# Kernel optimization log

Measured on AMD Instinct MI355X. Metric: run time of the kernel, lower is better.

Reference implementation:

```python
import jax, jax.numpy as jnp
import numpy as np

N, E, F, H = 20000, 320000, 128, 256   # nodes, edges, in-features, hidden
M, NQ = 4096, 2048                      # lsq rows, QP variables
LAMB_MAX = 2.0


def setup_inputs() -> dict:
    key = jax.random.key(0)
    ks = jax.random.split(key, 12)
    x = jax.random.normal(ks[0], (N, F), jnp.float32)
    edge_index = jax.random.randint(ks[1], (2, E), 0, N)
    A = jax.random.normal(ks[2], (M, NQ), jnp.float32) * 0.05
    b = jax.random.normal(ks[3], (M, 1), jnp.float32)
    feat_ids = jax.random.randint(ks[4], (NQ,), 0, N)
    x_prior = jax.random.uniform(ks[5], (NQ, 1), jnp.float32)
    lamb = jnp.ones((1,), jnp.float32)
    # ChebConv K=2 weights: one linear per Chebyshev order, plus bias
    W10 = jax.random.normal(ks[6], (F, H), jnp.float32) / np.sqrt(F)
    W11 = jax.random.normal(ks[7], (F, H), jnp.float32) / np.sqrt(F)
    b1 = jnp.zeros((H,), jnp.float32)
    W20 = jax.random.normal(ks[8], (H, 1), jnp.float32) / np.sqrt(H)
    W21 = jax.random.normal(ks[9], (H, 1), jnp.float32) / np.sqrt(H)
    b2 = jnp.zeros((1,), jnp.float32)
    return {"x": x, "edge_index": edge_index, "A": A, "b": b,
            "feat_ids": feat_ids, "x_prior": x_prior, "lamb": lamb,
            "W10": W10, "W11": W11, "b1": b1,
            "W20": W20, "W21": W21, "b2": b2}


def _cheb_conv(x, edge_index, W0, W1, bias, lam_max):
    """PyG ChebConv with K=2: out = x @ W0 + (2L/lam_max - I) x @ W1 + bias,
    L = I - D^{-1/2} A D^{-1/2}, via edge gather/scatter (no dense NxN)."""
    row, col = edge_index[0], edge_index[1]
    n = x.shape[0]
    deg = jax.ops.segment_sum(jnp.ones_like(row, dtype=x.dtype), row, num_segments=n)
    dinv = jnp.where(deg > 0, deg ** -0.5, 0.0)
    # normalized edge weight scaled by 2/lam_max, negated (off-diag of L_hat)
    w = -(2.0 / lam_max) * dinv[row] * dinv[col]              # [E]
    msg = jax.ops.segment_sum(w[:, None] * x[col], row, num_segments=n)
    Tx1 = msg + (2.0 / lam_max - 1.0) * x                      # diagonal of L_hat
    return x @ W0 + Tx1 @ W1 + bias


def reference(x, edge_index, A, b, feat_ids, x_prior, lamb,
              W10, W11, b1, W20, W21, b2):
    h = jax.nn.relu(_cheb_conv(x, edge_index, W10, W11, b1, LAMB_MAX))
    h = lamb[0] * jax.nn.relu(_cheb_conv(h, edge_index, W20, W21, b2, LAMB_MAX))
    hfold = h[feat_ids] + 1e-5                                 # [NQ, 1]
    q = hfold[:, 0]
    # QP: min 1/2 z^T Q z + p^T z with vacuous inequality (0*z <= 0.1) and no
    # equality constraints -> interior-point converges to unconstrained min.
    Q = A.T @ A + jnp.diag(q)                                  # [NQ, NQ]
    p = -(x_prior * hfold)[:, 0] - (b.T @ A)[0]                # [NQ]
    z = jnp.linalg.solve(Q, -p)                                # [NQ]
    return z[:, None]                                          # f.T -> [NQ, 1]
```

## Files before the change

### kernel.cpp

```cpp
#include <hip/hip_runtime.h>

#define N_NODES 20000
#define N_EDGES 320000
#define F_DIM   128
#define H_DIM   256
#define M_ROWS  4096
#define NQ      2048
#define NIT     18
#define MM_ROWS 20032

typedef __attribute__((ext_vector_type(8))) short short8;
typedef __attribute__((ext_vector_type(4))) float f32x4;


__device__ __forceinline__ float wred(float v) {
#pragma unroll
  for (int m = 32; m > 0; m >>= 1) v += __shfl_xor(v, m, 64);
  return v;
}

__device__ __forceinline__ float bred256(float v, float* lds) {
  v = wred(v);
  int w = threadIdx.x >> 6;
  if ((threadIdx.x & 63) == 0) lds[w] = v;
  __syncthreads();
  float tot = lds[0] + lds[1] + lds[2] + lds[3];
  __syncthreads();
  return tot;
}

__device__ __forceinline__ unsigned f2bf(float f) {
  unsigned u = __float_as_uint(f);
  unsigned r = u + 0x7fffu + ((u >> 16) & 1u);
  return r >> 16;
}
__device__ __forceinline__ float bflo(unsigned u) { return __uint_as_float(u << 16); }
__device__ __forceinline__ float bfhi(unsigned u) { return __uint_as_float(u & 0xffff0000u); }


__global__ __launch_bounds__(256) void k_deg(const int* __restrict__ ei, int* __restrict__ deg) {
  int e = blockIdx.x * 256 + threadIdx.x;
  if (e < N_EDGES) atomicAdd(&deg[ei[e]], 1);
}

__global__ __launch_bounds__(1024) void k_scan(const int* __restrict__ deg,
    int* __restrict__ rowstart, float* __restrict__ dinv) {
  __shared__ int part[1024];
  int t = threadIdx.x;
  const int chunk = (N_NODES + 1023) / 1024;
  int lo = t * chunk;
  int hi = lo + chunk; if (hi > N_NODES) hi = N_NODES;
  int s = 0;
  for (int i = lo; i < hi; ++i) {
    int d = deg[i];
    dinv[i] = d > 0 ? rsqrtf((float)d) : 0.f;
    s += d;
  }
  part[t] = s;
  __syncthreads();
  for (int off = 1; off < 1024; off <<= 1) {
    int v = part[t];
    int add = (t >= off) ? part[t - off] : 0;
    __syncthreads();
    part[t] = v + add;
    __syncthreads();
  }
  int base = (t > 0) ? part[t - 1] : 0;
  for (int i = lo; i < hi; ++i) { rowstart[i] = base; base += deg[i]; }
  if (t == 0) rowstart[N_NODES] = part[1023];
}

__global__ __launch_bounds__(256) void k_scatter(const int* __restrict__ ei,
    const int* __restrict__ rowstart, int* __restrict__ cursor,
    const float* __restrict__ dinv, int* __restrict__ cols, float* __restrict__ wvals) {
  int e = blockIdx.x * 256 + threadIdx.x;
  if (e >= N_EDGES) return;
  int r = ei[e];
  int c = ei[N_EDGES + e];
  int pos = rowstart[r] + atomicAdd(&cursor[r], 1);
  cols[pos] = c;
  wvals[pos] = -dinv[r] * dinv[c];
}

#define CONVX_BLKS (MM_ROWS * 16 / 256)

__global__ __launch_bounds__(256) void k_pack(const float* __restrict__ x,
    const float* __restrict__ W10, const float* __restrict__ W11,
    unsigned* __restrict__ xu, unsigned* __restrict__ Wtb) {
  int bx = blockIdx.x;
  if (bx < CONVX_BLKS) {
    int gid = bx * 256 + threadIdx.x;
    int row = gid >> 4;
    int q8 = gid & 15;
    uint4* xu4 = (uint4*)xu;
    if (row < N_NODES) {
      const float4* x4 = (const float4*)x;
      float4 a = x4[(size_t)row * 32 + q8 * 2];
      float4 b = x4[(size_t)row * 32 + q8 * 2 + 1];
      uint4 u;
      u.x = f2bf(a.x) | (f2bf(a.y) << 16);
      u.y = f2bf(a.z) | (f2bf(a.w) << 16);
      u.z = f2bf(b.x) | (f2bf(b.y) << 16);
      u.w = f2bf(b.z) | (f2bf(b.w) << 16);
      xu4[(size_t)row * 32 + q8] = u;
    } else {
      uint4 z = make_uint4(0, 0, 0, 0);
      xu4[(size_t)row * 32 + q8] = z;
      xu4[(size_t)row * 32 + 16 + q8] = z;
    }
  } else {
    int gid = (bx - CONVX_BLKS) * 256 + threadIdx.x;
    int n = gid >> 7;
    int u = gid & 127;
    int k0 = u * 2;
    float v0 = (k0 < 128) ? W10[(size_t)k0 * H_DIM + n]
                          : W11[(size_t)(k0 - 128) * H_DIM + n];
    float v1 = (k0 + 1 < 128) ? W10[(size_t)(k0 + 1) * H_DIM + n]
                              : W11[(size_t)(k0 - 127) * H_DIM + n];
    Wtb[(size_t)n * 128 + u] = f2bf(v0) | (f2bf(v1) << 16);
  }
}

__global__ __launch_bounds__(256) void k_msg1(const int* __restrict__ rowstart,
    const int* __restrict__ cols, const float* __restrict__ wvals,
    unsigned* __restrict__ xu) {
  int wid = (blockIdx.x * 256 + threadIdx.x) >> 6;
  int lane = threadIdx.x & 63;
  if (wid >= N_NODES) return;
  int s0 = rowstart[wid], s1 = rowstart[wid + 1];
  float2 acc = make_float2(0.f, 0.f);
  for (int e = s0; e < s1; ++e) {
    int c = cols[e];
    float w = wvals[e];
    unsigned u = xu[(size_t)c * 128 + lane];
    acc.x += w * bflo(u);
    acc.y += w * bfhi(u);
  }
  xu[(size_t)wid * 128 + 64 + lane] = f2bf(acc.x) | (f2bf(acc.y) << 16);
}


__device__ __forceinline__ void mm_ldfrag(short8* Af, short8* Bf,
    const unsigned* __restrict__ xurow, const unsigned* __restrict__ wrow, int kc) {
#pragma unroll
  for (int a = 0; a < 4; ++a)
    Af[a] = *(const short8*)(xurow + (size_t)a * 16 * 128 + kc * 16);
#pragma unroll
  for (int n = 0; n < 4; ++n)
    Bf[n] = *(const short8*)(wrow + (size_t)n * 16 * 128 + kc * 16);
}

__global__ __launch_bounds__(256) void k_mm(const unsigned* __restrict__ xu,
    const unsigned* __restrict__ Wtb, const float* __restrict__ b1,
    const float* __restrict__ W20, const float* __restrict__ W21,
    float* __restrict__ t, float* __restrict__ s) {
  const int row0 = blockIdx.x * 64;
  const int tid = threadIdx.x;
  const int w = tid >> 6, lane = tid & 63;
  const int colb = w * 64;
  const int frow = lane & 15, fqo = (lane >> 4) * 4;
  const int c16 = lane & 15, q4 = lane >> 4;

  f32x4 acc[4][4];
#pragma unroll
  for (int a = 0; a < 4; ++a)
#pragma unroll
    for (int b = 0; b < 4; ++b) {
      acc[a][b][0] = 0.f; acc[a][b][1] = 0.f;
      acc[a][b][2] = 0.f; acc[a][b][3] = 0.f;
    }

  const unsigned* xurow = xu + (size_t)(row0 + frow) * 128 + fqo;
  const unsigned* wrow  = Wtb + (size_t)(colb + frow) * 128 + fqo;

  short8 A0[4], B0[4], A1[4], B1[4];
  mm_ldfrag(A0, B0, xurow, wrow, 0);
#pragma unroll
  for (int kp = 0; kp < 4; ++kp) {
    const int kc = kp * 2;
    mm_ldfrag(A1, B1, xurow, wrow, kc + 1);
#pragma unroll
    for (int a = 0; a < 4; ++a)
#pragma unroll
      for (int n = 0; n < 4; ++n)
        acc[a][n] = __builtin_amdgcn_mfma_f32_16x16x32_bf16(A0[a], B0[n], acc[a][n], 0, 0, 0);
    if (kc + 2 < 8) mm_ldfrag(A0, B0, xurow, wrow, kc + 2);
#pragma unroll
    for (int a = 0; a < 4; ++a)
#pragma unroll
      for (int n = 0; n < 4; ++n)
        acc[a][n] = __builtin_amdgcn_mfma_f32_16x16x32_bf16(A1[a], B1[n], acc[a][n], 0, 0, 0);
  }

  float tp[4][4] = {}, sp[4][4] = {};
#pragma unroll
  for (int b2 = 0; b2 < 4; ++b2) {
    int gc = colb + b2 * 16 + c16;
    float w20 = W20[gc], w21 = W21[gc], bb = b1[gc];
#pragma unroll
    for (int a = 0; a < 4; ++a)
#pragma unroll
      for (int r = 0; r < 4; ++r) {
        float val = acc[a][b2][r] + bb;
        val = val > 0.f ? val : 0.f;
        tp[a][r] += val * w20;
        sp[a][r] += val * w21;
      }
  }
#pragma unroll
  for (int a = 0; a < 4; ++a)
#pragma unroll
    for (int r = 0; r < 4; ++r) {
#pragma unroll
      for (int m = 1; m < 16; m <<= 1) {
        tp[a][r] += __shfl_xor(tp[a][r], m, 64);
        sp[a][r] += __shfl_xor(sp[a][r], m, 64);
      }
    }
  if (c16 == 0) {
#pragma unroll
    for (int a = 0; a < 4; ++a)
#pragma unroll
      for (int r = 0; r < 4; ++r) {
        int gr = row0 + a * 16 + q4 * 4 + r;
        if (gr < N_NODES) {
          atomicAdd(&t[gr], tp[a][r]);
          atomicAdd(&s[gr], sp[a][r]);
        }
      }
  }
}


__global__ __launch_bounds__(256) void k_h2(const float* __restrict__ t,
    const float* __restrict__ s, const int* __restrict__ rowstart,
    const int* __restrict__ cols, const float* __restrict__ wvals,
    const float* __restrict__ lamb, const float* __restrict__ b2, float* __restrict__ h2) {
  int i = blockIdx.x * 256 + threadIdx.x;
  if (i >= N_NODES) return;
  float m = 0.f;
  int s0 = rowstart[i], s1 = rowstart[i + 1];
  for (int e = s0; e < s1; ++e) m += wvals[e] * s[cols[e]];
  float val = t[i] + m + b2[0];
  val = val > 0.f ? val : 0.f;
  h2[i] = lamb[0] * val;
}

__global__ __launch_bounds__(256) void k_prep(const float* __restrict__ A,
    const float* __restrict__ b, unsigned* __restrict__ Atu, float* __restrict__ btA_parts) {
  int jp = blockIdx.x * 256 + threadIdx.x;
  int k0 = blockIdx.y * 128;
  const float2* A2 = (const float2*)A;
  float acc0 = 0.f, acc1 = 0.f;
  for (int kk = 0; kk < 128; kk += 8) {
    float ax[8], ay[8];
#pragma unroll
    for (int i = 0; i < 8; ++i) {
      int k = k0 + kk + i;
      float2 a = A2[(size_t)k * 1024 + jp];
      float bk = b[k];
      acc0 += a.x * bk;
      acc1 += a.y * bk;
      ax[i] = a.x; ay[i] = a.y;
    }
    uint4 t0, t1;
    t0.x = f2bf(ax[0]) | (f2bf(ax[1]) << 16);
    t0.y = f2bf(ax[2]) | (f2bf(ax[3]) << 16);
    t0.z = f2bf(ax[4]) | (f2bf(ax[5]) << 16);
    t0.w = f2bf(ax[6]) | (f2bf(ax[7]) << 16);
    t1.x = f2bf(ay[0]) | (f2bf(ay[1]) << 16);
    t1.y = f2bf(ay[2]) | (f2bf(ay[3]) << 16);
    t1.z = f2bf(ay[4]) | (f2bf(ay[5]) << 16);
    t1.w = f2bf(ay[6]) | (f2bf(ay[7]) << 16);
    int uoff = (k0 + kk) >> 1;
    *(uint4*)(Atu + (size_t)(2 * jp) * 2048 + uoff) = t0;
    *(uint4*)(Atu + (size_t)(2 * jp + 1) * 2048 + uoff) = t1;
  }
  ((float2*)(btA_parts + (size_t)blockIdx.y * NQ))[jp] = make_float2(acc0, acc1);
}

__global__ __launch_bounds__(256) void k_qrhs(const float* __restrict__ h2,
    const int* __restrict__ feat_ids, const float* __restrict__ x_prior,
    const float* __restrict__ btA_parts, float* __restrict__ q, float* __restrict__ r) {
  int j = blockIdx.x * 256 + threadIdx.x;
  int f = feat_ids[j];
  float hf = h2[f] + 1e-5f;
  q[j] = hf;
  float bta = 0.f;
#pragma unroll
  for (int c = 0; c < 32; ++c) bta += btA_parts[(size_t)c * NQ + j];
  r[j] = x_prior[j] * hf + bta;
}

#define GR_ST 20
#define NTILE 136

__global__ __launch_bounds__(512) void k_gram(const unsigned* __restrict__ Atu,
                                              float* __restrict__ Gp) {
  __shared__ unsigned shA[128 * GR_ST];
  __shared__ unsigned shB[128 * GR_ST];
  const int bid = blockIdx.x;
  const int wid = (bid & 7) * 68 + (bid >> 3);
  const int tile = wid >> 2;
  const int kq = wid & 3;
  int uu = tile, bi = 0;
  while (uu >= 16 - bi) { uu -= 16 - bi; ++bi; }
  const int bj = bi + uu;
  const int i0 = bi * 128, j0 = bj * 128;
  const int tid = threadIdx.x;
  const int w = tid >> 6, lane = tid & 63;
  const int wr = (w >> 2) * 64, wc = (w & 3) * 32;
  const int srow = tid >> 2, suo = (tid & 3) * 4;
  const int frow = lane & 15, fqo = (lane >> 4) * 4;

  f32x4 acc[4][2];
#pragma unroll
  for (int a = 0; a < 4; ++a)
#pragma unroll
    for (int b = 0; b < 2; ++b) {
      acc[a][b][0] = 0.f; acc[a][b][1] = 0.f;
      acc[a][b][2] = 0.f; acc[a][b][3] = 0.f;
    }

  const unsigned* pa = Atu + (size_t)(i0 + srow) * 2048 + kq * 512 + suo;
  const unsigned* pb = Atu + (size_t)(j0 + srow) * 2048 + kq * 512 + suo;

  uint4 ra0 = *(const uint4*)(pa);
  uint4 rb0 = *(const uint4*)(pb);
  uint4 ra1 = *(const uint4*)(pa + 16);
  uint4 rb1 = *(const uint4*)(pb + 16);

  unsigned* as = shA + srow * GR_ST + suo;
  unsigned* bs = shB + srow * GR_ST + suo;

  for (int sp = 0; sp < 16; ++sp) {
    *(uint4*)as = ra0;
    *(uint4*)bs = rb0;
    if (sp < 15) {
      const int ku = (2 * sp + 2) * 16;
      ra0 = *(const uint4*)(pa + ku);
      rb0 = *(const uint4*)(pb + ku);
    }
    __syncthreads();
    {
      short8 af[4], bf[2];
#pragma unroll
      for (int a = 0; a < 4; ++a)
        af[a] = *(const short8*)(shA + (wr + a * 16 + frow) * GR_ST + fqo);
#pragma unroll
      for (int b2 = 0; b2 < 2; ++b2)
        bf[b2] = *(const short8*)(shB + (wc + b2 * 16 + frow) * GR_ST + fqo);
#pragma unroll
      for (int a = 0; a < 4; ++a)
#pragma unroll
        for (int b2 = 0; b2 < 2; ++b2)
          acc[a][b2] = __builtin_amdgcn_mfma_f32_16x16x32_bf16(af[a], bf[b2], acc[a][b2], 0, 0, 0);
    }
    __syncthreads();
    *(uint4*)as = ra1;
    *(uint4*)bs = rb1;
    if (sp < 15) {
      const int ku = (2 * sp + 3) * 16;
      ra1 = *(const uint4*)(pa + ku);
      rb1 = *(const uint4*)(pb + ku);
    }
    __syncthreads();
    {
      short8 af[4], bf[2];
#pragma unroll
      for (int a = 0; a < 4; ++a)
        af[a] = *(const short8*)(shA + (wr + a * 16 + frow) * GR_ST + fqo);
#pragma unroll
      for (int b2 = 0; b2 < 2; ++b2)
        bf[b2] = *(const short8*)(shB + (wc + b2 * 16 + frow) * GR_ST + fqo);
#pragma unroll
      for (int a = 0; a < 4; ++a)
#pragma unroll
        for (int b2 = 0; b2 < 2; ++b2)
          acc[a][b2] = __builtin_amdgcn_mfma_f32_16x16x32_bf16(af[a], bf[b2], acc[a][b2], 0, 0, 0);
    }
    __syncthreads();
  }

  const int q4 = lane >> 4, c16 = lane & 15;
  float* Gz = Gp + ((size_t)kq * NTILE + tile) * 16384;
#pragma unroll
  for (int a = 0; a < 4; ++a)
#pragma unroll
    for (int b2 = 0; b2 < 2; ++b2)
#pragma unroll
      for (int r = 0; r < 4; ++r) {
        int lr = wr + a * 16 + q4 * 4 + r;
        int lc = wc + b2 * 16 + c16;
        Gz[lr * 128 + lc] = acc[a][b2][r];
      }
}

#define GT_ST 131

__global__ __launch_bounds__(256) void k_gconv(const float* __restrict__ Gp,
    const float* __restrict__ q, unsigned* __restrict__ Gb, float* __restrict__ qcorr) {
  __shared__ unsigned short T[128 * GT_ST];
  int uu = blockIdx.x, bi = 0;
  while (uu >= 16 - bi) { uu -= 16 - bi; ++bi; }
  const int bj = bi + uu;
  const int tid = threadIdx.x;
  const int r = tid >> 1, ch = (tid & 1) * 64;
  const size_t tile = (size_t)blockIdx.x * 16384;
  const float4* P0 = (const float4*)(Gp + tile + r * 128 + ch);
  const float4* P1 = (const float4*)(Gp + (size_t)1 * NTILE * 16384 + tile + r * 128 + ch);
  const float4* P2 = (const float4*)(Gp + (size_t)2 * NTILE * 16384 + tile + r * 128 + ch);
  const float4* P3 = (const float4*)(Gp + (size_t)3 * NTILE * 16384 + tile + r * 128 + ch);
  const int gr = bi * 128 + r;
  const bool hasdiag = (bi == bj) && (r >= ch) && (r < ch + 64);
  unsigned uo[32];
#pragma unroll
  for (int j = 0; j < 16; ++j) {
    float4 a = P0[j], b = P1[j], c = P2[j], d = P3[j];
    float v0 = a.x + b.x + c.x + d.x;
    float v1 = a.y + b.y + c.y + d.y;
    float v2 = a.z + b.z + c.z + d.z;
    float v3 = a.w + b.w + c.w + d.w;
    const int c0 = ch + j * 4;
    if (hasdiag && (r - c0 >= 0) && (r - c0 < 4)) {
      float qv = q[gr];
      int dsel = r - c0;
      if (dsel == 0) v0 += qv;
      else if (dsel == 1) v1 += qv;
      else if (dsel == 2) v2 += qv;
      else v3 += qv;
      float vd = (dsel == 0) ? v0 : (dsel == 1) ? v1 : (dsel == 2) ? v2 : v3;
      qcorr[gr] = vd - bflo(f2bf(vd));
    }
    unsigned u0 = f2bf(v0) | (f2bf(v1) << 16);
    unsigned u1 = f2bf(v2) | (f2bf(v3) << 16);
    uo[2 * j] = u0;
    uo[2 * j + 1] = u1;
    T[r * GT_ST + c0]     = (unsigned short)(u0 & 0xffffu);
    T[r * GT_ST + c0 + 1] = (unsigned short)(u0 >> 16);
    T[r * GT_ST + c0 + 2] = (unsigned short)(u1 & 0xffffu);
    T[r * GT_ST + c0 + 3] = (unsigned short)(u1 >> 16);
  }
  uint4* dst = (uint4*)(Gb + (size_t)gr * 1024 + bj * 64 + (ch >> 1));
#pragma unroll
  for (int j = 0; j < 8; ++j) dst[j] = ((const uint4*)uo)[j];
  __syncthreads();
  if (bi != bj) {
    const int wv = tid >> 6, lane = tid & 63;
    for (int kk = 0; kk < 32; ++kk) {
      int rr = kk * 4 + wv;
      unsigned lo = T[(2 * lane) * GT_ST + rr];
      unsigned hi = T[(2 * lane + 1) * GT_ST + rr];
      Gb[(size_t)(bj * 128 + rr) * 1024 + bi * 64 + lane] = lo | (hi << 16);
    }
  }
}

__global__ __launch_bounds__(256) void k_cgG(int k, const unsigned* __restrict__ Gb,
    const float* __restrict__ qcorr,
    const float* __restrict__ r_old, float* __restrict__ r_new,
    const float* __restrict__ p_old, float* __restrict__ p_new,
    const float* __restrict__ Qp_in, float* __restrict__ Qp_out,
    float* __restrict__ xcg) {
  __shared__ float pshare[NQ];
  __shared__ float lds[4];
  const int tid = threadIdx.x, bid = blockIdx.x;
  const float4* r4 = (const float4*)r_old;
  float4 ra = r4[tid * 2], rb2 = r4[tid * 2 + 1];
  float pv[8];
  if (k == 0) {
    pv[0] = ra.x; pv[1] = ra.y; pv[2] = ra.z; pv[3] = ra.w;
    pv[4] = rb2.x; pv[5] = rb2.y; pv[6] = rb2.z; pv[7] = rb2.w;
    if (bid == 0) {
      ((float4*)p_new)[tid * 2] = ra;
      ((float4*)p_new)[tid * 2 + 1] = rb2;
    }
  } else {
    const float4* p4 = (const float4*)p_old;
    const float4* qp4 = (const float4*)Qp_in;
    float4 pa = p4[tid * 2], pb = p4[tid * 2 + 1];
    float4 qa = qp4[tid * 2], qb = qp4[tid * 2 + 1];
    float rr = ra.x * ra.x + ra.y * ra.y + ra.z * ra.z + ra.w * ra.w +
               rb2.x * rb2.x + rb2.y * rb2.y + rb2.z * rb2.z + rb2.w * rb2.w;
    float pap = pa.x * qa.x + pa.y * qa.y + pa.z * qa.z + pa.w * qa.w +
                pb.x * qb.x + pb.y * qb.y + pb.z * qb.z + pb.w * qb.w;
    rr = bred256(rr, lds);
    pap = bred256(pap, lds);
    float alpha = rr / pap;
    if (bid == 0) {
      float4* x4 = (float4*)xcg;
      float4 xa = x4[tid * 2], xb = x4[tid * 2 + 1];
      xa.x += alpha * pa.x; xa.y += alpha * pa.y;
      xa.z += alpha * pa.z; xa.w += alpha * pa.w;
      xb.x += alpha * pb.x; xb.y += alpha * pb.y;
      xb.z += alpha * pb.z; xb.w += alpha * pb.w;
      x4[tid * 2] = xa; x4[tid * 2 + 1] = xb;
    }
    ra.x -= alpha * qa.x; ra.y -= alpha * qa.y;
    ra.z -= alpha * qa.z; ra.w -= alpha * qa.w;
    rb2.x -= alpha * qb.x; rb2.y -= alpha * qb.y;
    rb2.z -= alpha * qb.z; rb2.w -= alpha * qb.w;
    float rrn = ra.x * ra.x + ra.y * ra.y + ra.z * ra.z + ra.w * ra.w +
                rb2.x * rb2.x + rb2.y * rb2.y + rb2.z * rb2.z + rb2.w * rb2.w;
    rrn = bred256(rrn, lds);
    float beta = rrn / rr;
    pv[0] = ra.x + beta * pa.x; pv[1] = ra.y + beta * pa.y;
    pv[2] = ra.z + beta * pa.z; pv[3] = ra.w + beta * pa.w;
    pv[4] = rb2.x + beta * pb.x; pv[5] = rb2.y + beta * pb.y;
    pv[6] = rb2.z + beta * pb.z; pv[7] = rb2.w + beta * pb.w;
    if (bid == 0) {
      ((float4*)r_new)[tid * 2] = ra;
      ((float4*)r_new)[tid * 2 + 1] = rb2;
      ((float4*)p_new)[tid * 2] = make_float4(pv[0], pv[1], pv[2], pv[3]);
      ((float4*)p_new)[tid * 2 + 1] = make_float4(pv[4], pv[5], pv[6], pv[7]);
    }
  }
  ((float4*)pshare)[tid * 2] = make_float4(pv[0], pv[1], pv[2], pv[3]);
  ((float4*)pshare)[tid * 2 + 1] = make_float4(pv[4], pv[5], pv[6], pv[7]);
  __syncthreads();
  const int w = tid >> 6, lane = tid & 63;
  const int row0 = bid * 8 + w * 2;
  const uint4* Gr0 = (const uint4*)(Gb + (size_t)row0 * 1024);
  const uint4* Gr1 = (const uint4*)(Gb + (size_t)(row0 + 1) * 1024);
  const float4* ps4 = (const float4*)pshare;
  float acc0 = 0.f, acc1 = 0.f;
#pragma unroll
  for (int c = 0; c < 4; ++c) {
    uint4 g0 = Gr0[c * 64 + lane];
    uint4 g1 = Gr1[c * 64 + lane];
    float4 pa = ps4[c * 128 + lane * 2];
    float4 pb = ps4[c * 128 + lane * 2 + 1];
    acc0 += bflo(g0.x) * pa.x + bfhi(g0.x) * pa.y;
    acc0 += bflo(g0.y) * pa.z + bfhi(g0.y) * pa.w;
    acc0 += bflo(g0.z) * pb.x + bfhi(g0.z) * pb.y;
    acc0 += bflo(g0.w) * pb.z + bfhi(g0.w) * pb.w;
    acc1 += bflo(g1.x) * pa.x + bfhi(g1.x) * pa.y;
    acc1 += bflo(g1.y) * pa.z + bfhi(g1.y) * pa.w;
    acc1 += bflo(g1.z) * pb.x + bfhi(g1.z) * pb.y;
    acc1 += bflo(g1.w) * pb.z + bfhi(g1.w) * pb.w;
  }
  acc0 = wred(acc0);
  acc1 = wred(acc1);
  if (lane == 0) {
    Qp_out[row0] = acc0 + qcorr[row0] * pshare[row0];
    Qp_out[row0 + 1] = acc1 + qcorr[row0 + 1] * pshare[row0 + 1];
  }
}

__global__ __launch_bounds__(256) void k_cgfin(const float* __restrict__ r_last,
    const float* __restrict__ p_last, const float* __restrict__ Qp,
    const float* __restrict__ xcg, float* __restrict__ out) {
  const int tid = threadIdx.x;
  const int lane = tid & 63;
  const float4* r4 = (const float4*)r_last;
  const float4* p4 = (const float4*)p_last;
  const float4* q4 = (const float4*)Qp;
  float rr = 0.f, pap = 0.f;
#pragma unroll
  for (int c = 0; c < 4; ++c) {
#pragma unroll
    for (int hh = 0; hh < 2; ++hh) {
      float4 rv = r4[c * 128 + lane * 2 + hh];
      float4 pv = p4[c * 128 + lane * 2 + hh];
      float4 qv = q4[c * 128 + lane * 2 + hh];
      rr += rv.x * rv.x + rv.y * rv.y + rv.z * rv.z + rv.w * rv.w;
      pap += pv.x * qv.x + pv.y * qv.y + pv.z * qv.z + pv.w * qv.w;
    }
  }
  rr = wred(rr);
  pap = wred(pap);
  float alpha = rr / pap;
  const float4* x4 = (const float4*)xcg;
  float4* o4 = (float4*)out;
#pragma unroll
  for (int hh = 0; hh < 2; ++hh) {
    int i4 = tid * 2 + hh;
    float4 xv = x4[i4];
    float4 pv = p4[i4];
    xv.x += alpha * pv.x; xv.y += alpha * pv.y;
    xv.z += alpha * pv.z; xv.w += alpha * pv.w;
    o4[i4] = xv;
  }
}


extern "C" void kernel_launch(void* const* d_in, const int* in_sizes, int n_in,
                              void* d_out, int out_size, void* d_ws, size_t ws_size,
                              hipStream_t stream) {
  const float* x      = (const float*)d_in[0];
  const int*   ei     = (const int*)d_in[1];
  const float* A      = (const float*)d_in[2];
  const float* b      = (const float*)d_in[3];
  const int*   fids   = (const int*)d_in[4];
  const float* xprior = (const float*)d_in[5];
  const float* lamb   = (const float*)d_in[6];
  const float* W10    = (const float*)d_in[7];
  const float* W11    = (const float*)d_in[8];
  const float* b1     = (const float*)d_in[9];
  const float* W20    = (const float*)d_in[10];
  const float* W21    = (const float*)d_in[11];
  const float* b2     = (const float*)d_in[12];
  float* out = (float*)d_out;

  char* base = (char*)d_ws;
  size_t o = 0;
  auto alloc = [&](size_t bytes) { size_t r = o; o = (o + bytes + 255) & ~size_t(255); return r; };

  size_t off_deg    = alloc(N_NODES * 4);
  size_t off_cursor = alloc(N_NODES * 4);
  size_t off_xcg    = alloc(NQ * 4);
  size_t off_t      = alloc(N_NODES * 4);
  size_t off_s      = alloc(N_NODES * 4);
  size_t zero_end   = o;
  size_t off_rowst  = alloc((N_NODES + 1) * 4);
  size_t off_dinv   = alloc(N_NODES * 4);
  size_t off_h2     = alloc(N_NODES * 4);
  size_t off_q      = alloc(NQ * 4);
  size_t off_r0     = alloc(NQ * 4);
  size_t off_r1     = alloc(NQ * 4);
  size_t off_p0     = alloc(NQ * 4);
  size_t off_p1     = alloc(NQ * 4);
  size_t off_Qp0    = alloc(NQ * 4);
  size_t off_Qp1    = alloc(NQ * 4);
  size_t off_qcorr  = alloc(NQ * 4);
  size_t off_btAp   = alloc(32 * NQ * 4);
  size_t off_Wtb    = alloc(256 * 128 * 4);
  size_t sz_cols  = (size_t)N_EDGES * 4 + 256;
  size_t sz_wvals = (size_t)N_EDGES * 4 + 256;
  size_t sz_xmsg  = (size_t)MM_ROWS * 256 * 2;
  size_t union_gnn = sz_cols + sz_wvals + sz_xmsg;
  size_t union_at  = (size_t)M_ROWS * NQ * 2;
  size_t off_union = alloc(union_gnn > union_at ? union_gnn : union_at);
  size_t off_Gp    = alloc((size_t)4 * NTILE * 16384 * 4);
  if (o > ws_size) return;

  int*   deg      = (int*)(base + off_deg);
  int*   cursor   = (int*)(base + off_cursor);
  float* xcg      = (float*)(base + off_xcg);
  float* t        = (float*)(base + off_t);
  float* s        = (float*)(base + off_s);
  int*   rowstart = (int*)(base + off_rowst);
  float* dinv     = (float*)(base + off_dinv);
  float* h2       = (float*)(base + off_h2);
  float* q        = (float*)(base + off_q);
  float* rb[2]    = {(float*)(base + off_r0), (float*)(base + off_r1)};
  float* pg[2]    = {(float*)(base + off_p0), (float*)(base + off_p1)};
  float* Qpb[2]   = {(float*)(base + off_Qp0), (float*)(base + off_Qp1)};
  float* qcorr    = (float*)(base + off_qcorr);
  float* btA_parts = (float*)(base + off_btAp);
  unsigned* Wtb   = (unsigned*)(base + off_Wtb);
  int*   cols     = (int*)(base + off_union);
  float* wvals    = (float*)(base + off_union + sz_cols);
  unsigned* xmsgb = (unsigned*)(base + off_union + sz_cols + sz_wvals);
  unsigned* Atu   = (unsigned*)(base + off_union);
  unsigned* Gb    = (unsigned*)(base + off_union);
  float* Gp       = (float*)(base + off_Gp);

  hipMemsetAsync(d_ws, 0, zero_end, stream);

  k_deg<<<(N_EDGES + 255) / 256, 256, 0, stream>>>(ei, deg);
  k_scan<<<1, 1024, 0, stream>>>(deg, rowstart, dinv);
  k_scatter<<<(N_EDGES + 255) / 256, 256, 0, stream>>>(ei, rowstart, cursor, dinv, cols, wvals);

  k_pack<<<CONVX_BLKS + 128, 256, 0, stream>>>(x, W10, W11, xmsgb, Wtb);
  k_msg1<<<N_NODES / 4, 256, 0, stream>>>(rowstart, cols, wvals, xmsgb);
  k_mm<<<MM_ROWS / 64, 256, 0, stream>>>(xmsgb, Wtb, b1, W20, W21, t, s);
  k_h2<<<(N_NODES + 255) / 256, 256, 0, stream>>>(t, s, rowstart, cols, wvals, lamb, b2, h2);

  k_prep<<<dim3(4, 32), 256, 0, stream>>>(A, b, Atu, btA_parts);
  k_qrhs<<<NQ / 256, 256, 0, stream>>>(h2, fids, xprior, btA_parts, q, rb[0]);
  k_gram<<<544, 512, 0, stream>>>(Atu, Gp);
  k_gconv<<<NTILE, 256, 0, stream>>>(Gp, q, Gb, qcorr);

  k_cgG<<<256, 256, 0, stream>>>(0, Gb, qcorr, rb[0], rb[0], pg[0], pg[0],
                                 Qpb[1], Qpb[0], xcg);
  for (int k = 1; k < NIT; ++k) {
    k_cgG<<<256, 256, 0, stream>>>(k, Gb, qcorr, rb[(k - 1) & 1], rb[k & 1],
                                   pg[(k - 1) & 1], pg[k & 1],
                                   Qpb[(k - 1) & 1], Qpb[k & 1], xcg);
  }
  k_cgfin<<<1, 256, 0, stream>>>(rb[(NIT - 1) & 1], pg[(NIT - 1) & 1],
                                 Qpb[(NIT - 1) & 1], xcg, out);
}
```

Measured before the change: 406.2 us.

## Fuse CG iteration kernels into one cooperative persistent kernel with grid sync

Replaces the 18 per-iteration CG kernel launches and the final update launch with a single cooperative kernel. It loops over the iterations internally and uses grid-wide synchronization between them. The goal is to remove per-launch overhead and the gaps between dependent small kernels. In exchange, each iteration pays for a grid barrier plus a thread fence, which on AMD GPUs can cost about as much as a launch boundary.

```diff
diff --git a/kernel.cpp b/kernel.cpp
--- a/kernel.cpp
+++ b/kernel.cpp
@@ -1,4 +1,7 @@
 #include <hip/hip_runtime.h>
+#include <hip/hip_cooperative_groups.h>
+
+namespace cg = cooperative_groups;
 
 #define N_NODES 20000
 #define N_EDGES 320000
@@ -456,130 +459,144 @@
   }
 }
 
-__global__ __launch_bounds__(256) void k_cgG(int k, const unsigned* __restrict__ Gb,
+__global__ __launch_bounds__(256) void k_cg_all(const unsigned* __restrict__ Gb,
     const float* __restrict__ qcorr,
-    const float* __restrict__ r_old, float* __restrict__ r_new,
-    const float* __restrict__ p_old, float* __restrict__ p_new,
-    const float* __restrict__ Qp_in, float* __restrict__ Qp_out,
-    float* __restrict__ xcg) {
+    float* __restrict__ r0b, float* __restrict__ r1b,
+    float* __restrict__ p0b, float* __restrict__ p1b,
+    float* __restrict__ q0b, float* __restrict__ q1b,
+    float* __restrict__ xcg, float* __restrict__ out) {
+  cg::grid_group grid = cg::this_grid();
   __shared__ float pshare[NQ];
   __shared__ float lds[4];
   const int tid = threadIdx.x, bid = blockIdx.x;
-  const float4* r4 = (const float4*)r_old;
-  float4 ra = r4[tid * 2], rb2 = r4[tid * 2 + 1];
-  float pv[8];
-  if (k == 0) {
-    pv[0] = ra.x; pv[1] = ra.y; pv[2] = ra.z; pv[3] = ra.w;
-    pv[4] = rb2.x; pv[5] = rb2.y; pv[6] = rb2.z; pv[7] = rb2.w;
-    if (bid == 0) {
-      ((float4*)p_new)[tid * 2] = ra;
-      ((float4*)p_new)[tid * 2 + 1] = rb2;
-    }
-  } else {
-    const float4* p4 = (const float4*)p_old;
-    const float4* qp4 = (const float4*)Qp_in;
-    float4 pa = p4[tid * 2], pb = p4[tid * 2 + 1];
-    float4 qa = qp4[tid * 2], qb = qp4[tid * 2 + 1];
-    float rr = ra.x * ra.x + ra.y * ra.y + ra.z * ra.z + ra.w * ra.w +
-               rb2.x * rb2.x + rb2.y * rb2.y + rb2.z * rb2.z + rb2.w * rb2.w;
-    float pap = pa.x * qa.x + pa.y * qa.y + pa.z * qa.z + pa.w * qa.w +
-                pb.x * qb.x + pb.y * qb.y + pb.z * qb.z + pb.w * qb.w;
-    rr = bred256(rr, lds);
-    pap = bred256(pap, lds);
-    float alpha = rr / pap;
-    if (bid == 0) {
-      float4* x4 = (float4*)xcg;
-      float4 xa = x4[tid * 2], xb = x4[tid * 2 + 1];
-      xa.x += alpha * pa.x; xa.y += alpha * pa.y;
-      xa.z += alpha * pa.z; xa.w += alpha * pa.w;
-      xb.x += alpha * pb.x; xb.y += alpha * pb.y;
-      xb.z += alpha * pb.z; xb.w += alpha * pb.w;
-      x4[tid * 2] = xa; x4[tid * 2 + 1] = xb;
-    }
-    ra.x -= alpha * qa.x; ra.y -= alpha * qa.y;
-    ra.z -= alpha * qa.z; ra.w -= alpha * qa.w;
-    rb2.x -= alpha * qb.x; rb2.y -= alpha * qb.y;
-    rb2.z -= alpha * qb.z; rb2.w -= alpha * qb.w;
-    float rrn = ra.x * ra.x + ra.y * ra.y + ra.z * ra.z + ra.w * ra.w +
-                rb2.x * rb2.x + rb2.y * rb2.y + rb2.z * rb2.z + rb2.w * rb2.w;
-    rrn = bred256(rrn, lds);
-    float beta = rrn / rr;
-    pv[0] = ra.x + beta * pa.x; pv[1] = ra.y + beta * pa.y;
-    pv[2] = ra.z + beta * pa.z; pv[3] = ra.w + beta * pa.w;
-    pv[4] = rb2.x + beta * pb.x; pv[5] = rb2.y + beta * pb.y;
-    pv[6] = rb2.z + beta * pb.z; pv[7] = rb2.w + beta * pb.w;
-    if (bid == 0) {
-      ((float4*)r_new)[tid * 2] = ra;
-      ((float4*)r_new)[tid * 2 + 1] = rb2;
-      ((float4*)p_new)[tid * 2] = make_float4(pv[0], pv[1], pv[2], pv[3]);
-      ((float4*)p_new)[tid * 2 + 1] = make_float4(pv[4], pv[5], pv[6], pv[7]);
-    }
-  }
-  ((float4*)pshare)[tid * 2] = make_float4(pv[0], pv[1], pv[2], pv[3]);
-  ((float4*)pshare)[tid * 2 + 1] = make_float4(pv[4], pv[5], pv[6], pv[7]);
-  __syncthreads();
   const int w = tid >> 6, lane = tid & 63;
   const int row0 = bid * 8 + w * 2;
   const uint4* Gr0 = (const uint4*)(Gb + (size_t)row0 * 1024);
   const uint4* Gr1 = (const uint4*)(Gb + (size_t)(row0 + 1) * 1024);
-  const float4* ps4 = (const float4*)pshare;
-  float acc0 = 0.f, acc1 = 0.f;
-#pragma unroll
-  for (int c = 0; c < 4; ++c) {
-    uint4 g0 = Gr0[c * 64 + lane];
-    uint4 g1 = Gr1[c * 64 + lane];
-    float4 pa = ps4[c * 128 + lane * 2];
-    float4 pb = ps4[c * 128 + lane * 2 + 1];
-    acc0 += bflo(g0.x) * pa.x + bfhi(g0.x) * pa.y;
-    acc0 += bflo(g0.y) * pa.z + bfhi(g0.y) * pa.w;
-    acc0 += bflo(g0.z) * pb.x + bfhi(g0.z) * pb.y;
-    acc0 += bflo(g0.w) * pb.z + bfhi(g0.w) * pb.w;
-    acc1 += bflo(g1.x) * pa.x + bfhi(g1.x) * pa.y;
-    acc1 += bflo(g1.y) * pa.z + bfhi(g1.y) * pa.w;
-    acc1 += bflo(g1.z) * pb.x + bfhi(g1.z) * pb.y;
-    acc1 += bflo(g1.w) * pb.z + bfhi(g1.w) * pb.w;
-  }
-  acc0 = wred(acc0);
-  acc1 = wred(acc1);
-  if (lane == 0) {
-    Qp_out[row0] = acc0 + qcorr[row0] * pshare[row0];
-    Qp_out[row0 + 1] = acc1 + qcorr[row0 + 1] * pshare[row0 + 1];
-  }
-}
-
-__global__ __launch_bounds__(256) void k_cgfin(const float* __restrict__ r_last,
-    const float* __restrict__ p_last, const float* __restrict__ Qp,
-    const float* __restrict__ xcg, float* __restrict__ out) {
-  const int tid = threadIdx.x;
-  const int lane = tid & 63;
-  const float4* r4 = (const float4*)r_last;
-  const float4* p4 = (const float4*)p_last;
-  const float4* q4 = (const float4*)Qp;
-  float rr = 0.f, pap = 0.f;
-#pragma unroll
-  for (int c = 0; c < 4; ++c) {
+
+  for (int k = 0; k < NIT; ++k) {
+    const int io = (k == 0) ? 0 : ((k - 1) & 1);
+    const int in_ = k & 1;
+    const float* r_old = io ? r1b : r0b;
+    float* r_new = in_ ? r1b : r0b;
+    const float* p_old = io ? p1b : p0b;
+    float* p_new = in_ ? p1b : p0b;
+    const float* Qp_in = io ? q1b : q0b;
+    float* Qp_out = in_ ? q1b : q0b;
+
+    const float4* r4 = (const float4*)r_old;
+    float4 ra = r4[tid * 2], rb2 = r4[tid * 2 + 1];
+    float pv[8];
+    if (k == 0) {
+      pv[0] = ra.x; pv[1] = ra.y; pv[2] = ra.z; pv[3] = ra.w;
+      pv[4] = rb2.x; pv[5] = rb2.y; pv[6] = rb2.z; pv[7] = rb2.w;
+      if (bid == 0) {
+        ((float4*)p_new)[tid * 2] = ra;
+        ((float4*)p_new)[tid * 2 + 1] = rb2;
+      }
+    } else {
+      const float4* p4 = (const float4*)p_old;
+      const float4* qp4 = (const float4*)Qp_in;
+      float4 pa = p4[tid * 2], pb = p4[tid * 2 + 1];
+      float4 qa = qp4[tid * 2], qb = qp4[tid * 2 + 1];
+      float rr = ra.x * ra.x + ra.y * ra.y + ra.z * ra.z + ra.w * ra.w +
+                 rb2.x * rb2.x + rb2.y * rb2.y + rb2.z * rb2.z + rb2.w * rb2.w;
+      float pap = pa.x * qa.x + pa.y * qa.y + pa.z * qa.z + pa.w * qa.w +
+                  pb.x * qb.x + pb.y * qb.y + pb.z * qb.z + pb.w * qb.w;
+      rr = bred256(rr, lds);
+      pap = bred256(pap, lds);
+      float alpha = rr / pap;
+      if (bid == 0) {
+        float4* x4 = (float4*)xcg;
+        float4 xa = x4[tid * 2], xb = x4[tid * 2 + 1];
+        xa.x += alpha * pa.x; xa.y += alpha * pa.y;
+        xa.z += alpha * pa.z; xa.w += alpha * pa.w;
+        xb.x += alpha * pb.x; xb.y += alpha * pb.y;
+        xb.z += alpha * pb.z; xb.w += alpha * pb.w;
+        x4[tid * 2] = xa; x4[tid * 2 + 1] = xb;
+      }
+      ra.x -= alpha * qa.x; ra.y -= alpha * qa.y;
+      ra.z -= alpha * qa.z; ra.w -= alpha * qa.w;
+      rb2.x -= alpha * qb.x; rb2.y -= alpha * qb.y;
+      rb2.z -= alpha * qb.z; rb2.w -= alpha * qb.w;
+      float rrn = ra.x * ra.x + ra.y * ra.y + ra.z * ra.z + ra.w * ra.w +
+                  rb2.x * rb2.x + rb2.y * rb2.y + rb2.z * rb2.z + rb2.w * rb2.w;
+      rrn = bred256(rrn, lds);
+      float beta = rrn / rr;
+      pv[0] = ra.x + beta * pa.x; pv[1] = ra.y + beta * pa.y;
+      pv[2] = ra.z + beta * pa.z; pv[3] = ra.w + beta * pa.w;
+      pv[4] = rb2.x + beta * pb.x; pv[5] = rb2.y + beta * pb.y;
+      pv[6] = rb2.z + beta * pb.z; pv[7] = rb2.w + beta * pb.w;
+      if (bid == 0) {
+        ((float4*)r_new)[tid * 2] = ra;
+        ((float4*)r_new)[tid * 2 + 1] = rb2;
+        ((float4*)p_new)[tid * 2] = make_float4(pv[0], pv[1], pv[2], pv[3]);
+        ((float4*)p_new)[tid * 2 + 1] = make_float4(pv[4], pv[5], pv[6], pv[7]);
+      }
+    }
+    ((float4*)pshare)[tid * 2] = make_float4(pv[0], pv[1], pv[2], pv[3]);
+    ((float4*)pshare)[tid * 2 + 1] = make_float4(pv[4], pv[5], pv[6], pv[7]);
+    __syncthreads();
+    const float4* ps4 = (const float4*)pshare;
+    float acc0 = 0.f, acc1 = 0.f;
+#pragma unroll
+    for (int c = 0; c < 4; ++c) {
+      uint4 g0 = Gr0[c * 64 + lane];
+      uint4 g1 = Gr1[c * 64 + lane];
+      float4 pa = ps4[c * 128 + lane * 2];
+      float4 pb = ps4[c * 128 + lane * 2 + 1];
+      acc0 += bflo(g0.x) * pa.x + bfhi(g0.x) * pa.y;
+      acc0 += bflo(g0.y) * pa.z + bfhi(g0.y) * pa.w;
+      acc0 += bflo(g0.z) * pb.x + bfhi(g0.z) * pb.y;
+      acc0 += bflo(g0.w) * pb.z + bfhi(g0.w) * pb.w;
+      acc1 += bflo(g1.x) * pa.x + bfhi(g1.x) * pa.y;
+      acc1 += bflo(g1.y) * pa.z + bfhi(g1.y) * pa.w;
+      acc1 += bflo(g1.z) * pb.x + bfhi(g1.z) * pb.y;
+      acc1 += bflo(g1.w) * pb.z + bfhi(g1.w) * pb.w;
+    }
+    acc0 = wred(acc0);
+    acc1 = wred(acc1);
+    if (lane == 0) {
+      Qp_out[row0] = acc0 + qcorr[row0] * pshare[row0];
+      Qp_out[row0 + 1] = acc1 + qcorr[row0 + 1] * pshare[row0 + 1];
+    }
+    __threadfence();
+    grid.sync();
+  }
+
+  if (bid == 0) {
+    const float* r_last = ((NIT - 1) & 1) ? r1b : r0b;
+    const float* p_last = ((NIT - 1) & 1) ? p1b : p0b;
+    const float* Qp = ((NIT - 1) & 1) ? q1b : q0b;
+    const float4* r4 = (const float4*)r_last;
+    const float4* p4 = (const float4*)p_last;
+    const float4* q4 = (const float4*)Qp;
+    float rr = 0.f, pap = 0.f;
+#pragma unroll
+    for (int c = 0; c < 4; ++c) {
+#pragma unroll
+      for (int hh = 0; hh < 2; ++hh) {
+        float4 rv = r4[c * 128 + lane * 2 + hh];
+        float4 pv = p4[c * 128 + lane * 2 + hh];
+        float4 qv = q4[c * 128 + lane * 2 + hh];
+        rr += rv.x * rv.x + rv.y * rv.y + rv.z * rv.z + rv.w * rv.w;
+        pap += pv.x * qv.x + pv.y * qv.y + pv.z * qv.z + pv.w * qv.w;
+      }
+    }
+    rr = wred(rr);
+    pap = wred(pap);
+    float alpha = rr / pap;
+    const float4* x4 = (const float4*)xcg;
+    float4* o4 = (float4*)out;
 #pragma unroll
     for (int hh = 0; hh < 2; ++hh) {
-      float4 rv = r4[c * 128 + lane * 2 + hh];
-      float4 pv = p4[c * 128 + lane * 2 + hh];
-      float4 qv = q4[c * 128 + lane * 2 + hh];
-      rr += rv.x * rv.x + rv.y * rv.y + rv.z * rv.z + rv.w * rv.w;
-      pap += pv.x * qv.x + pv.y * qv.y + pv.z * qv.z + pv.w * qv.w;
-    }
-  }
-  rr = wred(rr);
-  pap = wred(pap);
-  float alpha = rr / pap;
-  const float4* x4 = (const float4*)xcg;
-  float4* o4 = (float4*)out;
-#pragma unroll
-  for (int hh = 0; hh < 2; ++hh) {
-    int i4 = tid * 2 + hh;
-    float4 xv = x4[i4];
-    float4 pv = p4[i4];
-    xv.x += alpha * pv.x; xv.y += alpha * pv.y;
-    xv.z += alpha * pv.z; xv.w += alpha * pv.w;
-    o4[i4] = xv;
+      int i4 = tid * 2 + hh;
+      float4 xv = x4[i4];
+      float4 pv = p4[i4];
+      xv.x += alpha * pv.x; xv.y += alpha * pv.y;
+      xv.z += alpha * pv.z; xv.w += alpha * pv.w;
+      o4[i4] = xv;
+    }
   }
 }
 
@@ -672,13 +689,11 @@
   k_gram<<<544, 512, 0, stream>>>(Atu, Gp);
   k_gconv<<<NTILE, 256, 0, stream>>>(Gp, q, Gb, qcorr);
 
-  k_cgG<<<256, 256, 0, stream>>>(0, Gb, qcorr, rb[0], rb[0], pg[0], pg[0],
-                                 Qpb[1], Qpb[0], xcg);
-  for (int k = 1; k < NIT; ++k) {
-    k_cgG<<<256, 256, 0, stream>>>(k, Gb, qcorr, rb[(k - 1) & 1], rb[k & 1],
-                                   pg[(k - 1) & 1], pg[k & 1],
-                                   Qpb[(k - 1) & 1], Qpb[k & 1], xcg);
-  }
-  k_cgfin<<<1, 256, 0, stream>>>(rb[(NIT - 1) & 1], pg[(NIT - 1) & 1],
-                                 Qpb[(NIT - 1) & 1], xcg, out);
-}
+  void* cgargs[] = {(void*)&Gb, (void*)&qcorr,
+                    (void*)&rb[0], (void*)&rb[1],
+                    (void*)&pg[0], (void*)&pg[1],
+                    (void*)&Qpb[0], (void*)&Qpb[1],
+                    (void*)&xcg, (void*)&out};
+  hipLaunchCooperativeKernel((const void*)k_cg_all, dim3(256), dim3(256),
+                             cgargs, 0u, stream);
+}
```

Result: slower. 1.259 ms (+210.0%).
